# Kernel optimization log

Measured on AMD Instinct MI355X. Metric: run time of the kernel, lower is better.

Reference implementation:

```python
import jax, jax.numpy as jnp
from jax import lax
import numpy as np

LOG2PI = float(np.log(2.0 * np.pi))
FMIN = float(np.finfo(np.float32).min)


def seq_mask(lengths, maxlen):
    # [B, maxlen] float32
    return (jnp.arange(maxlen)[None] < lengths[:, None]).astype(jnp.float32)


def monotonic_alignment_search(ll, attnmask):
    """Faithful port of GlowTTS.monotonic_alignment_search.
    ll, attnmask: [B, T, S] float32. Returns [B, T, S] float32.
    Note: replicates the source exactly, including stacking backtracked rows
    in descending-j (append) order before masking, as written in the TF code.
    """
    B, T, S = ll.shape
    x_range = jnp.arange(S)[None]  # [1, S]

    def fwd(prob, j_and_ll):
        j, ll_j = j_and_ll  # ll_j: [B, S]
        prev = jnp.pad(prob, ((0, 0), (1, 0)), constant_values=-jnp.inf)[:, :-1]
        max_mask = prob >= prev                       # [B, S] bool
        prob_max = jnp.where(max_mask, prob, prev)
        prob_new = jnp.where(x_range <= j, prob_max + ll_j, FMIN)
        return prob_new, max_mask

    _, direction = lax.scan(fwd, jnp.zeros((B, S), jnp.float32),
                            (jnp.arange(T), jnp.transpose(ll, (1, 0, 2))))
    direction = jnp.transpose(direction, (1, 0, 2)).astype(jnp.int32)  # [B, T, S]
    direction = jnp.where(attnmask.astype(bool), direction, 1)

    index = attnmask[:, 0].sum(axis=-1).astype(jnp.int32) - 1  # [B]
    brange = jnp.arange(B)

    def bwd(index, j):
        attn_j = jax.nn.one_hot(index, S, dtype=jnp.float32)  # drops index<0 like scatter_nd
        d = direction[brange, j, index]                       # [B]
        return index + d - 1, attn_j

    _, attn = lax.scan(bwd, index, jnp.arange(T)[::-1])
    attn = jnp.transpose(attn, (1, 0, 2))  # [B, T, S], rows in append order
    return attn * attnmask


def setup_inputs() -> dict:
    key = jax.random.key(0)
    k1, k2, k3, k4, k5 = jax.random.split(key, 5)
    B, T, S, C = 32, 1200, 384, 160
    latent = jax.random.normal(k1, (B, T, C), dtype=jnp.float32)
    mean = jax.random.normal(k2, (B, S, C), dtype=jnp.float32)
    logdur = jax.random.normal(k3, (B, S), dtype=jnp.float32)
    textlen = jax.random.randint(k4, (B,), S // 2, S + 1).astype(jnp.int32)
    mellen = jax.random.randint(k5, (B,), T // 2, T + 1).astype(jnp.int32)
    return {"latent": latent, "mean": mean, "logdur": logdur,
            "textlen": textlen, "mellen": mellen}


def reference(latent, mean, logdur, textlen, mellen):
    B, T, C = latent.shape
    S = mean.shape[1]
    mask = seq_mask(textlen, S)     # [B, S]
    melmask = seq_mask(mellen, T)   # [B, T]
    attnmask = melmask[..., None] * mask[:, None]  # [B, T, S]

    # pairwise squared distance (cdist via matmul + reduce_sum)
    dist = (jnp.sum(jnp.square(latent), axis=-1, keepdims=True)
            - 2.0 * jnp.einsum('btc,bsc->bts', latent, mean)
            + jnp.sum(jnp.square(mean), axis=-1)[:, None])
    ll = -0.5 * (LOG2PI + dist) * attnmask

    attn = lax.stop_gradient(monotonic_alignment_search(ll, attnmask))
    aligned = jnp.einsum('bts,bsc->btc', attn, mean)  # [B, T, C]

    # negative log-likelihood (dlogdet of the flow omitted: constant here)
    nll = 0.5 * (LOG2PI + jnp.sum(jnp.square(latent - aligned), axis=(1, 2)))
    nll = jnp.mean(nll / (mellen * C).astype(jnp.float32))

    gtdur = jnp.log(jnp.maximum(jnp.sum(attn, axis=1), 1e-05)) * mask
    durloss = jnp.sum(jnp.square(logdur - gtdur), axis=-1) / mellen.astype(jnp.float32)
    durloss = jnp.mean(durloss)

    loss = nll + durloss
    return loss, attn
```

## Files before the change

kernel.cpp:

```cpp
#include <hip/hip_runtime.h>
#include <math.h>

#define LOG2PI 1.8378770664093453f
#define F32MIN (-3.4028234663852886e38f)
#define SMAX 384
#define NW 38

__global__ __launch_bounds__(64) void k_sums(
    const float* __restrict__ latent, const float* __restrict__ mean,
    float* __restrict__ lx2, float* __restrict__ lm2, int BT, int BS, int C) {
  int row = blockIdx.x;
  int lane = threadIdx.x;
  const float* src;
  float* dst;
  if (row < BT) { src = latent + (size_t)row * C; dst = lx2 + row; }
  else          { src = mean + (size_t)(row - BT) * C; dst = lm2 + (row - BT); }
  float s = 0.f;
  for (int c = lane; c < C; c += 64) { float v = src[c]; s += v * v; }
  #pragma unroll
  for (int off = 32; off; off >>= 1) s += __shfl_down(s, off);
  if (lane == 0) *dst = s;
}

__global__ __launch_bounds__(256) void k_scores(
    const float* __restrict__ latent, const float* __restrict__ mean,
    const float* __restrict__ lx2, const float* __restrict__ lm2,
    const int* __restrict__ textlen, const int* __restrict__ mellen,
    float* __restrict__ ll, int T, int S, int C) {
  int b  = blockIdx.z;
  int t0 = blockIdx.x * 64;
  int s0 = blockIdx.y * 64;
  int mel = mellen[b], txt = textlen[b];
  int tid = threadIdx.x;
  int ty = tid >> 4, tx = tid & 15;
  float* out = ll + ((size_t)b * T + t0) * S + s0;

  if (t0 >= mel || s0 >= txt) {
    float4 z = make_float4(0.f, 0.f, 0.f, 0.f);
    #pragma unroll
    for (int i = 0; i < 4; ++i) {
      int tl = ty * 4 + i;
      if (t0 + tl < T) *(float4*)(out + (size_t)tl * S + tx * 4) = z;
    }
    return;
  }

  __shared__ float At[16][64];
  __shared__ float Bt[16][64];
  float acc[4][4] = {};

  const float* Ab = latent + ((size_t)b * T + t0) * C;
  const float* Bb = mean + ((size_t)b * S + s0) * C;

  for (int kk = 0; kk < C; kk += 16) {
    int r  = tid >> 2;
    int cg = tid & 3;
    float4 a = (t0 + r < T) ? *(const float4*)(Ab + (size_t)r * C + kk + cg * 4)
                            : make_float4(0.f, 0.f, 0.f, 0.f);
    float4 bm = *(const float4*)(Bb + (size_t)r * C + kk + cg * 4);
    At[cg * 4 + 0][r] = a.x;  At[cg * 4 + 1][r] = a.y;
    At[cg * 4 + 2][r] = a.z;  At[cg * 4 + 3][r] = a.w;
    Bt[cg * 4 + 0][r] = bm.x; Bt[cg * 4 + 1][r] = bm.y;
    Bt[cg * 4 + 2][r] = bm.z; Bt[cg * 4 + 3][r] = bm.w;
    __syncthreads();
    #pragma unroll
    for (int k = 0; k < 16; ++k) {
      float4 a4 = *(const float4*)&At[k][ty * 4];
      float4 b4 = *(const float4*)&Bt[k][tx * 4];
      float av[4] = {a4.x, a4.y, a4.z, a4.w};
      float bv[4] = {b4.x, b4.y, b4.z, b4.w};
      #pragma unroll
      for (int i = 0; i < 4; ++i)
        #pragma unroll
        for (int j = 0; j < 4; ++j)
          acc[i][j] = fmaf(av[i], bv[j], acc[i][j]);
    }
    __syncthreads();
  }

  #pragma unroll
  for (int i = 0; i < 4; ++i) {
    int t = t0 + ty * 4 + i;
    if (t >= T) continue;
    float lx = lx2[(size_t)b * T + t];
    float4 o;
    float* po = &o.x;
    #pragma unroll
    for (int j = 0; j < 4; ++j) {
      int s = s0 + tx * 4 + j;
      float d = lx - 2.f * acc[i][j] + lm2[(size_t)b * S + s];
      float v = -0.5f * (LOG2PI + d);
      po[j] = (t < mel && s < txt) ? v : 0.f;
    }
    *(float4*)(out + (size_t)(ty * 4 + i) * S + tx * 4) = o;
  }
}

__device__ __forceinline__ float dpp_shr1_neginf(float x) {
  int r = __builtin_amdgcn_update_dpp(
      __float_as_int(-INFINITY), __float_as_int(x),
      0x138 , 0xf, 0xf, false);
  return __int_as_float(r);
}

template <bool MASKED>
__device__ __forceinline__ void mas_step(
    int t, int sbase, int r, const float2 A0, const float2 A1, const float2 A2,
    float& p0, float& p1, float& p2, float& p3, float& p4, float& p5,
    unsigned& a0, unsigned& a1, unsigned& a2, unsigned& a3, unsigned& a4,
    unsigned& a5) {
  float l0 = A0.x, l1 = A0.y, l2 = A1.x, l3 = A1.y, l4 = A2.x, l5 = A2.y;
  float pm1 = dpp_shr1_neginf(p5);
  bool c0 = p0 >= pm1, c1 = p1 >= p0, c2 = p2 >= p1;
  bool c3 = p3 >= p2,  c4 = p4 >= p3, c5 = p5 >= p4;
  float m0 = c0 ? p0 : pm1, m1 = c1 ? p1 : p0, m2 = c2 ? p2 : p1;
  float m3 = c3 ? p3 : p2,  m4 = c4 ? p4 : p3, m5 = c5 ? p5 : p4;
  a0 |= (unsigned)c0 << r; a1 |= (unsigned)c1 << r; a2 |= (unsigned)c2 << r;
  a3 |= (unsigned)c3 << r; a4 |= (unsigned)c4 << r; a5 |= (unsigned)c5 << r;
  if (MASKED) {
    p0 = (sbase + 0 <= t) ? m0 + l0 : F32MIN;
    p1 = (sbase + 1 <= t) ? m1 + l1 : F32MIN;
    p2 = (sbase + 2 <= t) ? m2 + l2 : F32MIN;
    p3 = (sbase + 3 <= t) ? m3 + l3 : F32MIN;
    p4 = (sbase + 4 <= t) ? m4 + l4 : F32MIN;
    p5 = (sbase + 5 <= t) ? m5 + l5 : F32MIN;
  } else {
    p0 = m0 + l0; p1 = m1 + l1; p2 = m2 + l2;
    p3 = m3 + l3; p4 = m4 + l4; p5 = m5 + l5;
  }
}

template <bool MASKED, int ROWS>
__device__ __forceinline__ void scan_chunk_lds(
    const float* __restrict__ rcur, int t0, int sbase,
    float& p0, float& p1, float& p2, float& p3, float& p4, float& p5,
    unsigned* __restrict__ dirT, int cw) {
  unsigned a0 = 0, a1 = 0, a2 = 0, a3 = 0, a4 = 0, a5 = 0;
  const float2* q = (const float2*)(rcur + sbase);
  float2 A0 = q[0], A1 = q[1], A2 = q[2];
  #pragma unroll 1
  for (int r = 0; r < ROWS; r += 2) {
    const float2* qb = q + (size_t)(r + 1) * 192;
    float2 B0 = qb[0], B1 = qb[1], B2 = qb[2];
    mas_step<MASKED>(t0 + r, sbase, r, A0, A1, A2,
                     p0, p1, p2, p3, p4, p5, a0, a1, a2, a3, a4, a5);
    int rn = (r + 2 < ROWS) ? (r + 2) : (ROWS - 1);
    const float2* qa = q + (size_t)rn * 192;
    A0 = qa[0]; A1 = qa[1]; A2 = qa[2];
    mas_step<MASKED>(t0 + r + 1, sbase, r + 1, B0, B1, B2,
                     p0, p1, p2, p3, p4, p5, a0, a1, a2, a3, a4, a5);
  }
  unsigned* dcol = dirT + (unsigned)sbase * NW + cw;
  dcol[0] = a0; dcol[NW] = a1; dcol[2 * NW] = a2;
  dcol[3 * NW] = a3; dcol[4 * NW] = a4; dcol[5 * NW] = a5;
}

__global__ __launch_bounds__(256, 1) void k_scan(
    const float* __restrict__ ll, const int* __restrict__ textlen,
    const int* __restrict__ mellen, int* __restrict__ pathidx, int T, int S) {
  int b = blockIdx.x;
  int tid = threadIdx.x;
  int lane = tid & 63;
  __shared__ float rows[2][32][SMAX];
  __shared__ unsigned dirT[SMAX * NW];

  const float* llb = ll + (size_t)b * T * S;
  int mel = mellen[b], txt = textlen[b];
  int sbase = lane * 6;
  int nfull = T / 32;
  int nch = (T + 31) / 32;
  float p0 = 0.f, p1 = 0.f, p2 = 0.f, p3 = 0.f, p4 = 0.f, p5 = 0.f;

  if (tid >= 64) {
    int lid = tid - 64;
    const float4* g = (const float4*)llb;
    float4* d = (float4*)&rows[0][0][0];
    #pragma unroll
    for (int k = 0; k < 16; ++k) d[k * 192 + lid] = g[k * 192 + lid];
  }
  __syncthreads();

  for (int c = 0; c < nch; ++c) {
    if (tid >= 64) {
      int nxt = c + 1;
      if (nxt < nch) {
        int lid = tid - 64;
        const float4* g = (const float4*)(llb + (size_t)nxt * 32 * S);
        float4* d = (float4*)&rows[nxt & 1][0][0];
        if (nxt < nfull) {
          float4 stg[16];
          #pragma unroll
          for (int k = 0; k < 16; ++k) stg[k] = g[k * 192 + lid];
          #pragma unroll
          for (int k = 0; k < 16; ++k) d[k * 192 + lid] = stg[k];
        } else {
          float4 stg[8];
          #pragma unroll
          for (int k = 0; k < 8; ++k) stg[k] = g[k * 192 + lid];
          #pragma unroll
          for (int k = 0; k < 8; ++k) d[k * 192 + lid] = stg[k];
        }
      }
    } else {
      const float* rc = &rows[c & 1][0][0];
      int t0 = c * 32;
      if (c < nfull) {
        if (t0 < S)
          scan_chunk_lds<true, 32>(rc, t0, sbase, p0, p1, p2, p3, p4, p5, dirT, c);
        else
          scan_chunk_lds<false, 32>(rc, t0, sbase, p0, p1, p2, p3, p4, p5, dirT, c);
      } else {
        scan_chunk_lds<false, 16>(rc, t0, sbase, p0, p1, p2, p3, p4, p5, dirT, c);
      }
    }
    __syncthreads();
  }

  if (tid >= 64) return;

  size_t base = (size_t)b * T;
  int k0 = T - mel;
  for (int k = lane; k < k0; k += 64) pathidx[base + k] = txt - 1;

  if (lane == 0) {
    int i = txt - 1;
    int j = mel - 1;
    unsigned w = ~0u;
    bool reload = true;
    for (int k = k0; k < T; ++k) {
      pathidx[base + k] = i;
      if (reload) {
        int ii = (i < 0) ? i + S : i;
        ii = (ii < 0) ? 0 : ii;
        w = (ii < txt) ? dirT[ii * NW + (j >> 5)] : ~0u;
      }
      int d = (int)((w >> (j & 31)) & 1u);
      reload = (d == 0) | ((j & 31) == 0);
      i += d - 1;
      --j;
    }
  }
}

__global__ __launch_bounds__(256) void k_scatter(
    float* __restrict__ attn, const int* __restrict__ pathidx,
    const int* __restrict__ textlen, const int* __restrict__ mellen,
    int B, int T, int S) {
  size_t idx = ((size_t)blockIdx.x * blockDim.x + threadIdx.x) * 4;
  size_t total = (size_t)B * T * S;
  if (idx >= total) return;
  int s = (int)(idx % S);
  size_t row = idx / S;
  int b = (int)(row / T);
  int k = (int)(row % T);
  int pi = pathidx[row];
  int mel = mellen[b], txt = textlen[b];
  float4 o = make_float4(0.f, 0.f, 0.f, 0.f);
  if (k < mel && pi >= 0 && pi < S && pi < txt && pi >= s && pi < s + 4)
    (&o.x)[pi - s] = 1.f;
  *(float4*)(attn + idx) = o;
}

__global__ __launch_bounds__(256) void k_rowloss(
    const float* __restrict__ latent, const float* __restrict__ mean,
    const int* __restrict__ pathidx, const int* __restrict__ textlen,
    const int* __restrict__ mellen, float* __restrict__ rowsum,
    int T, int S, int C) {
  int row = blockIdx.x * 4 + (threadIdx.x >> 6);
  int lane = threadIdx.x & 63;
  int b = row / T, k = row % T;
  int pi = pathidx[row];
  int mel = mellen[b], txt = textlen[b];
  bool on = (k < mel) && (pi >= 0) && (pi < S) && (pi < txt);
  const float* L = latent + (size_t)row * C;
  const float* M = mean + ((size_t)b * S + (on ? pi : 0)) * C;
  float s = 0.f;
  for (int c = lane; c < C; c += 64) {
    float d = L[c] - (on ? M[c] : 0.f);
    s += d * d;
  }
  #pragma unroll
  for (int off = 32; off; off >>= 1) s += __shfl_down(s, off);
  if (lane == 0) rowsum[row] = s;
}

__global__ __launch_bounds__(256) void k_batch(
    const float* __restrict__ rowsum, const int* __restrict__ pathidx,
    const float* __restrict__ logdur, const int* __restrict__ textlen,
    const int* __restrict__ mellen, float* __restrict__ nllc,
    float* __restrict__ durc, int T, int S, int C) {
  int b = blockIdx.x;
  int tid = threadIdx.x;
  __shared__ int hist[512];
  __shared__ float red[256];
  int mel = mellen[b], txt = textlen[b];
  for (int s = tid; s < S; s += 256) hist[s] = 0;
  __syncthreads();
  for (int k = tid; k < T; k += 256) {
    int pi = pathidx[(size_t)b * T + k];
    if (k < mel && pi >= 0 && pi < S && pi < txt) atomicAdd(&hist[pi], 1);
  }
  __syncthreads();
  float part = 0.f;
  for (int s = tid; s < S; s += 256) {
    float cnt = (float)hist[s];
    float gt = logf(fmaxf(cnt, 1e-5f));
    gt = (s < txt) ? gt : 0.f;
    float d = logdur[(size_t)b * S + s] - gt;
    part += d * d;
  }
  red[tid] = part; __syncthreads();
  #pragma unroll
  for (int off = 128; off; off >>= 1) {
    if (tid < off) red[tid] += red[tid + off];
    __syncthreads();
  }
  if (tid == 0) durc[b] = red[0] / (float)mel;
  __syncthreads();
  part = 0.f;
  for (int k = tid; k < T; k += 256) part += rowsum[(size_t)b * T + k];
  red[tid] = part; __syncthreads();
  #pragma unroll
  for (int off = 128; off; off >>= 1) {
    if (tid < off) red[tid] += red[tid + off];
    __syncthreads();
  }
  if (tid == 0) nllc[b] = 0.5f * (LOG2PI + red[0]) / ((float)mel * (float)C);
}

__global__ __launch_bounds__(64) void k_final(
    const float* __restrict__ nllc, const float* __restrict__ durc,
    float* __restrict__ out, int B) {
  int lane = threadIdx.x;
  float v = (lane < B) ? (nllc[lane] + durc[lane]) : 0.f;
  #pragma unroll
  for (int off = 32; off; off >>= 1) v += __shfl_down(v, off);
  if (lane == 0) out[0] = v / (float)B;
}

extern "C" void kernel_launch(void* const* d_in, const int* in_sizes, int n_in,
                              void* d_out, int out_size, void* d_ws, size_t ws_size,
                              hipStream_t stream) {
  (void)n_in; (void)out_size; (void)ws_size;
  const float* latent = (const float*)d_in[0];
  const float* mean   = (const float*)d_in[1];
  const float* logdur = (const float*)d_in[2];
  const int*   textlen = (const int*)d_in[3];
  const int*   mellen  = (const int*)d_in[4];

  int B = in_sizes[3];
  int S = in_sizes[2] / B;
  int C = in_sizes[1] / (B * S);
  int T = in_sizes[0] / (B * C);

  float* out = (float*)d_out;
  float* ll = out + 1;

  char* ws = (char*)d_ws;
  float* lx2    = (float*)ws;
  float* lm2    = lx2 + (size_t)B * T;
  int*   pathidx = (int*)(lm2 + (size_t)B * S);
  float* rowsum  = (float*)(pathidx + (size_t)B * T);
  float* nllc    = rowsum + (size_t)B * T;
  float* durc    = nllc + B;

  k_sums<<<B * T + B * S, 64, 0, stream>>>(latent, mean, lx2, lm2, B * T, B * S, C);

  dim3 g2((T + 63) / 64, (S + 63) / 64, B);
  k_scores<<<g2, 256, 0, stream>>>(latent, mean, lx2, lm2, textlen, mellen, ll, T, S, C);

  k_scan<<<B, 256, 0, stream>>>(ll, textlen, mellen, pathidx, T, S);

  size_t total = (size_t)B * T * S;
  k_scatter<<<(int)((total / 4 + 255) / 256), 256, 0, stream>>>(ll, pathidx, textlen, mellen, B, T, S);

  k_rowloss<<<(B * T) / 4, 256, 0, stream>>>(latent, mean, pathidx, textlen, mellen, rowsum, T, S, C);

  k_batch<<<B, 256, 0, stream>>>(rowsum, pathidx, logdur, textlen, mellen, nllc, durc, T, S, C);

  k_final<<<1, 64, 0, stream>>>(nllc, durc, out, B);
}
```

Measured before the change: 324.9 us.

## Skip unreachable score tiles, truncate scan at mel length, fuse scatter with row loss

Result: faster. 311.5 us (-4.1%).

```diff
diff --git a/kernel.cpp b/kernel.cpp
--- a/kernel.cpp
+++ b/kernel.cpp
@@ -35,15 +35,7 @@
   int ty = tid >> 4, tx = tid & 15;
   float* out = ll + ((size_t)b * T + t0) * S + s0;
 
-  if (t0 >= mel || s0 >= txt) {
-    float4 z = make_float4(0.f, 0.f, 0.f, 0.f);
-    #pragma unroll
-    for (int i = 0; i < 4; ++i) {
-      int tl = ty * 4 + i;
-      if (t0 + tl < T) *(float4*)(out + (size_t)tl * S + tx * 4) = z;
-    }
-    return;
-  }
+  if (t0 >= mel || s0 >= txt || s0 > t0 + 63) return;
 
   __shared__ float At[16][64];
   __shared__ float Bt[16][64];
@@ -169,6 +161,8 @@
   int sbase = lane * 6;
   int nfull = T / 32;
   int nch = (T + 31) / 32;
+  int nchb = (mel + 31) / 32;
+  if (nchb > nch) nchb = nch;
   float p0 = 0.f, p1 = 0.f, p2 = 0.f, p3 = 0.f, p4 = 0.f, p5 = 0.f;
 
   if (tid >= 64) {
@@ -180,10 +174,10 @@
   }
   __syncthreads();
 
-  for (int c = 0; c < nch; ++c) {
+  for (int c = 0; c < nchb; ++c) {
     if (tid >= 64) {
       int nxt = c + 1;
-      if (nxt < nch) {
+      if (nxt < nchb) {
         int lid = tid - 64;
         const float4* g = (const float4*)(llb + (size_t)nxt * 32 * S);
         float4* d = (float4*)&rows[nxt & 1][0][0];
@@ -204,11 +198,10 @@
     } else {
       const float* rc = &rows[c & 1][0][0];
       int t0 = c * 32;
-      if (c < nfull) {
-        if (t0 < S)
-          scan_chunk_lds<true, 32>(rc, t0, sbase, p0, p1, p2, p3, p4, p5, dirT, c);
-        else
-          scan_chunk_lds<false, 32>(rc, t0, sbase, p0, p1, p2, p3, p4, p5, dirT, c);
+      if (c < 12) {
+        scan_chunk_lds<true, 32>(rc, t0, sbase, p0, p1, p2, p3, p4, p5, dirT, c);
+      } else if (c < nfull) {
+        scan_chunk_lds<false, 32>(rc, t0, sbase, p0, p1, p2, p3, p4, p5, dirT, c);
       } else {
         scan_chunk_lds<false, 16>(rc, t0, sbase, p0, p1, p2, p3, p4, p5, dirT, c);
       }
@@ -242,36 +235,26 @@
   }
 }
 
-__global__ __launch_bounds__(256) void k_scatter(
-    float* __restrict__ attn, const int* __restrict__ pathidx,
+__global__ __launch_bounds__(256) void k_scatrow(
+    float* __restrict__ attn, const float* __restrict__ latent,
+    const float* __restrict__ mean, const int* __restrict__ pathidx,
     const int* __restrict__ textlen, const int* __restrict__ mellen,
-    int B, int T, int S) {
-  size_t idx = ((size_t)blockIdx.x * blockDim.x + threadIdx.x) * 4;
-  size_t total = (size_t)B * T * S;
-  if (idx >= total) return;
-  int s = (int)(idx % S);
-  size_t row = idx / S;
-  int b = (int)(row / T);
-  int k = (int)(row % T);
-  int pi = pathidx[row];
-  int mel = mellen[b], txt = textlen[b];
-  float4 o = make_float4(0.f, 0.f, 0.f, 0.f);
-  if (k < mel && pi >= 0 && pi < S && pi < txt && pi >= s && pi < s + 4)
-    (&o.x)[pi - s] = 1.f;
-  *(float4*)(attn + idx) = o;
-}
-
-__global__ __launch_bounds__(256) void k_rowloss(
-    const float* __restrict__ latent, const float* __restrict__ mean,
-    const int* __restrict__ pathidx, const int* __restrict__ textlen,
-    const int* __restrict__ mellen, float* __restrict__ rowsum,
-    int T, int S, int C) {
+    float* __restrict__ rowsum, int T, int S, int C) {
   int row = blockIdx.x * 4 + (threadIdx.x >> 6);
   int lane = threadIdx.x & 63;
   int b = row / T, k = row % T;
   int pi = pathidx[row];
   int mel = mellen[b], txt = textlen[b];
   bool on = (k < mel) && (pi >= 0) && (pi < S) && (pi < txt);
+
+  float4* arow = (float4*)(attn + (size_t)row * S);
+  int nf4 = S >> 2;
+  for (int q = lane; q < nf4; q += 64) {
+    float4 v = make_float4(0.f, 0.f, 0.f, 0.f);
+    if (on && (pi >> 2) == q) (&v.x)[pi & 3] = 1.f;
+    arow[q] = v;
+  }
+
   const float* L = latent + (size_t)row * C;
   const float* M = mean + ((size_t)b * S + (on ? pi : 0)) * C;
   float s = 0.f;
@@ -371,10 +354,8 @@
 
   k_scan<<<B, 256, 0, stream>>>(ll, textlen, mellen, pathidx, T, S);
 
-  size_t total = (size_t)B * T * S;
-  k_scatter<<<(int)((total / 4 + 255) / 256), 256, 0, stream>>>(ll, pathidx, textlen, mellen, B, T, S);
-
-  k_rowloss<<<(B * T) / 4, 256, 0, stream>>>(latent, mean, pathidx, textlen, mellen, rowsum, T, S, C);
+  k_scatrow<<<(B * T) / 4, 256, 0, stream>>>(ll, latent, mean, pathidx, textlen,
+                                             mellen, rowsum, T, S, C);
 
   k_batch<<<B, 256, 0, stream>>>(rowsum, pathidx, logdur, textlen, mellen, nllc, durc, T, S, C);
 
```
